# Kernel optimization log

Measured on AMD Instinct MI355X. Metric: run time of the kernel, lower is better.

Reference implementation:

```python
import jax, jax.numpy as jnp
import numpy as np

EPS = 1e-12  # F.normalize default eps
TOPK = 3

def _l2norm_c(x):
    # normalize over channel axis 1 of [b,c,h,w]
    n = jnp.sqrt(jnp.sum(x * x, axis=1, keepdims=True))
    return x / jnp.maximum(n, EPS)

def _topk_axis1(x, k):
    # torch.topk(x, k, dim=-3) on [b, N, h, w] -> values [b, k, h, w]
    t = jnp.moveaxis(x, 1, -1)            # [b,h,w,N]
    vals, _ = jax.lax.top_k(t, k)         # [b,h,w,k]
    return jnp.moveaxis(vals, -1, 1)      # [b,k,h,w]

def setup_inputs() -> dict:
    key = jax.random.key(0)
    k1, k2 = jax.random.split(key)
    b, c, h, w = 4, 256, 64, 64
    xp = jax.random.normal(k1, (b, c, h, w), dtype=jnp.float32)
    xq = jax.random.normal(k2, (b, c, h, w), dtype=jnp.float32)
    alpha = jnp.float32(10.0)  # learned scalar parameter
    return {"xp": xp, "xq": xq, "alpha": alpha}

def reference(xp, xq, alpha):
    b, c, h1, w1 = xp.shape
    _, _, h2, w2 = xq.shape
    xpn = _l2norm_c(xp)
    xqn = _l2norm_c(xq)
    # [b, h1*w1, c] @ [b, c, h2*w2] -> [b, N1, N2]
    p = jnp.transpose(xpn, (0, 2, 3, 1)).reshape(b, h1 * w1, c)
    q = xqn.reshape(b, c, h2 * w2)
    x_aff = jnp.matmul(p, q)
    s = x_aff * alpha
    x_c = jax.nn.softmax(s, axis=-1) * jax.nn.softmax(s, axis=-2)
    # row-major reshape matches torch .view semantics
    xc_o_q = x_c.reshape(b, h1 * w1, h2, w2)
    valq = _topk_axis1(xc_o_q, TOPK)
    xc_o_p = jnp.moveaxis(xc_o_q, 1, -1).reshape(b, h2 * w2, h1, w1)
    valp = _topk_axis1(xc_o_p, TOPK)
    return (valp, valq, xc_o_p, xc_o_q)
```

## Files before the change

kernel.cpp:

```cpp
#include <hip/hip_runtime.h>
#include <cstdint>
#include <cstddef>

#define B_ 4
#define C_ 256
#define N_ 4096
#define BN_TOT (B_ * N_)

typedef _Float16 f16x8 __attribute__((ext_vector_type(8)));
typedef _Float16 f16x4 __attribute__((ext_vector_type(4)));
typedef float f32x4 __attribute__((ext_vector_type(4)));

__global__ __launch_bounds__(256) void norms_kernel(const float* __restrict__ xp,
                                                    const float* __restrict__ xq,
                                                    float* __restrict__ invp,
                                                    float* __restrict__ invq) {
  int idx = blockIdx.x * 256 + threadIdx.x;
  int tensor = idx >> 14;
  int rem = idx & 16383;
  const float* p = (tensor ? xq : xp) + (size_t)(rem >> 12) * C_ * N_ + (rem & 4095);
  float ss = 0.f;
#pragma unroll 16
  for (int ch = 0; ch < C_; ++ch) {
    float v = p[(size_t)ch * N_];
    ss = fmaf(v, v, ss);
  }
  float inv = 1.0f / fmaxf(sqrtf(ss), 1e-12f);
  (tensor ? invq : invp)[rem] = inv;
}

__global__ __launch_bounds__(256) void convert_kernel(const float* __restrict__ xp,
                                                      const float* __restrict__ xq,
                                                      const float* __restrict__ invp,
                                                      const float* __restrict__ invq,
                                                      _Float16* __restrict__ ph,
                                                      _Float16* __restrict__ pl,
                                                      _Float16* __restrict__ qh,
                                                      _Float16* __restrict__ ql) {
  __shared__ _Float16 ht[64][72];
  __shared__ _Float16 lt[64][72];
  const int tensor = blockIdx.z & 1;
  const int b = blockIdx.z >> 1;
  const int i0 = blockIdx.x * 64;
  const int c0 = blockIdx.y * 64;
  const int tid = threadIdx.x;
  const int si = tid & 15;
  const int sc = tid >> 4;
  const float* x = (tensor ? xq : xp) + (size_t)b * C_ * N_;
  const float* inv = (tensor ? invq : invp) + b * N_;
  _Float16* oh = (tensor ? qh : ph) + (size_t)b * N_ * C_;
  _Float16* ol = (tensor ? ql : pl) + (size_t)b * N_ * C_;

  float4 iv = *(const float4*)&inv[i0 + si * 4];

  _Float16 hv[4][4], lv[4][4];
#pragma unroll
  for (int rr = 0; rr < 4; ++rr) {
    float4 v = *(const float4*)&x[(size_t)(c0 + sc * 4 + rr) * N_ + i0 + si * 4];
    float f0 = v.x * iv.x, f1 = v.y * iv.y, f2 = v.z * iv.z, f3 = v.w * iv.w;
    _Float16 h0 = (_Float16)f0, h1 = (_Float16)f1, h2 = (_Float16)f2, h3 = (_Float16)f3;
    hv[rr][0] = h0; lv[rr][0] = (_Float16)((f0 - (float)h0) * 1024.f);
    hv[rr][1] = h1; lv[rr][1] = (_Float16)((f1 - (float)h1) * 1024.f);
    hv[rr][2] = h2; lv[rr][2] = (_Float16)((f2 - (float)h2) * 1024.f);
    hv[rr][3] = h3; lv[rr][3] = (_Float16)((f3 - (float)h3) * 1024.f);
  }
#pragma unroll
  for (int u = 0; u < 4; ++u) {
    f16x4 th = {hv[0][u], hv[1][u], hv[2][u], hv[3][u]};
    f16x4 tl = {lv[0][u], lv[1][u], lv[2][u], lv[3][u]};
    *(f16x4*)&ht[si * 4 + u][sc * 4] = th;
    *(f16x4*)&lt[si * 4 + u][sc * 4] = tl;
  }
  __syncthreads();
  const int ir = tid >> 2;
  const int ch = tid & 3;
  f16x8 h0 = *(const f16x8*)&ht[ir][ch * 16];
  f16x8 h1 = *(const f16x8*)&ht[ir][ch * 16 + 8];
  f16x8 l0 = *(const f16x8*)&lt[ir][ch * 16];
  f16x8 l1 = *(const f16x8*)&lt[ir][ch * 16 + 8];
  _Float16* po = oh + (size_t)(i0 + ir) * C_ + c0 + ch * 16;
  *(f16x8*)po = h0;
  *(f16x8*)(po + 8) = h1;
  _Float16* po2 = ol + (size_t)(i0 + ir) * C_ + c0 + ch * 16;
  *(f16x8*)po2 = l0;
  *(f16x8*)(po2 + 8) = l1;
}

__global__ __launch_bounds__(256, 2) void gemm_mfma_kernel(
    const _Float16* __restrict__ ph, const _Float16* __restrict__ pl,
    const _Float16* __restrict__ qh, const _Float16* __restrict__ ql,
    const float* __restrict__ alpha_p,
    float* __restrict__ e_out,
    float* __restrict__ rowsum, float* __restrict__ colsum) {
  __shared__ _Float16 Ah[128][40];
  __shared__ _Float16 Al[128][40];
  __shared__ _Float16 Bh[128][40];
  __shared__ _Float16 Bl[128][40];
  __shared__ float redr[2][128];
  __shared__ float redc[2][128];

  const int b = blockIdx.z;
  const int i0 = blockIdx.y * 128;
  const int j0 = blockIdx.x * 128;
  const int tid = threadIdx.x;
  const int lane = tid & 63;
  const int wave = tid >> 6;
  const int wr = wave >> 1;
  const int wc = wave & 1;

  const size_t tb = (size_t)b * N_ * C_;
  const _Float16* pAh = ph + tb + (size_t)(i0 + (tid >> 1)) * C_ + (tid & 1) * 16;
  const _Float16* pAl = pl + tb + (size_t)(i0 + (tid >> 1)) * C_ + (tid & 1) * 16;
  const _Float16* pBh = qh + tb + (size_t)(j0 + (tid >> 1)) * C_ + (tid & 1) * 16;
  const _Float16* pBl = ql + tb + (size_t)(j0 + (tid >> 1)) * C_ + (tid & 1) * 16;

  _Float16* wAh = &Ah[tid >> 1][(tid & 1) * 16];
  _Float16* wAl = &Al[tid >> 1][(tid & 1) * 16];
  _Float16* wBh = &Bh[tid >> 1][(tid & 1) * 16];
  _Float16* wBl = &Bl[tid >> 1][(tid & 1) * 16];

  f32x4 acc_hh[4][4], acc_m[4][4];
#pragma unroll
  for (int m = 0; m < 4; ++m)
#pragma unroll
    for (int n = 0; n < 4; ++n) {
      acc_hh[m][n] = (f32x4){0.f, 0.f, 0.f, 0.f};
      acc_m[m][n] = (f32x4){0.f, 0.f, 0.f, 0.f};
    }

  const int frow = lane & 15;
  const int fk = (lane >> 4) * 8;

  for (int k0 = 0; k0 < C_; k0 += 32) {
    f16x8 ra0 = *(const f16x8*)(pAh + k0);
    f16x8 ra1 = *(const f16x8*)(pAh + k0 + 8);
    f16x8 rb0 = *(const f16x8*)(pAl + k0);
    f16x8 rb1 = *(const f16x8*)(pAl + k0 + 8);
    f16x8 rc0 = *(const f16x8*)(pBh + k0);
    f16x8 rc1 = *(const f16x8*)(pBh + k0 + 8);
    f16x8 rd0 = *(const f16x8*)(pBl + k0);
    f16x8 rd1 = *(const f16x8*)(pBl + k0 + 8);
    __syncthreads();
    *(f16x8*)wAh = ra0; *(f16x8*)(wAh + 8) = ra1;
    *(f16x8*)wAl = rb0; *(f16x8*)(wAl + 8) = rb1;
    *(f16x8*)wBh = rc0; *(f16x8*)(wBh + 8) = rc1;
    *(f16x8*)wBl = rd0; *(f16x8*)(wBl + 8) = rd1;
    __syncthreads();

    f16x8 fah[4], fal[4], fbh[4], fbl[4];
#pragma unroll
    for (int m = 0; m < 4; ++m) {
      fah[m] = *(const f16x8*)&Ah[wr * 64 + m * 16 + frow][fk];
      fal[m] = *(const f16x8*)&Al[wr * 64 + m * 16 + frow][fk];
    }
#pragma unroll
    for (int n = 0; n < 4; ++n) {
      fbh[n] = *(const f16x8*)&Bh[wc * 64 + n * 16 + frow][fk];
      fbl[n] = *(const f16x8*)&Bl[wc * 64 + n * 16 + frow][fk];
    }
#pragma unroll
    for (int m = 0; m < 4; ++m)
#pragma unroll
      for (int n = 0; n < 4; ++n) {
        acc_hh[m][n] = __builtin_amdgcn_mfma_f32_16x16x32_f16(fah[m], fbh[n], acc_hh[m][n], 0, 0, 0);
        acc_m[m][n]  = __builtin_amdgcn_mfma_f32_16x16x32_f16(fah[m], fbl[n], acc_m[m][n], 0, 0, 0);
        acc_m[m][n]  = __builtin_amdgcn_mfma_f32_16x16x32_f16(fal[m], fbh[n], acc_m[m][n], 0, 0, 0);
      }
  }

  const float al = alpha_p[0];
  float rowp[4][4];
  float colp[4];
#pragma unroll
  for (int m = 0; m < 4; ++m)
#pragma unroll
    for (int r = 0; r < 4; ++r) rowp[m][r] = 0.f;
#pragma unroll
  for (int n = 0; n < 4; ++n) colp[n] = 0.f;

  const int rbase = i0 + wr * 64;
  const int cbase = j0 + wc * 64;
  const int rlane = (lane >> 4) * 4;
  const int clane = lane & 15;

#pragma unroll
  for (int m = 0; m < 4; ++m)
#pragma unroll
    for (int n = 0; n < 4; ++n) {
      f32x4 dh = acc_hh[m][n];
      f32x4 dm = acc_m[m][n];
#pragma unroll
      for (int reg = 0; reg < 4; ++reg) {
        float dot = dh[reg] + dm[reg] * (1.f / 1024.f);
        float e = __expf(al * dot);
        int row = rbase + m * 16 + rlane + reg;
        int col = cbase + n * 16 + clane;
        e_out[(size_t)(b * N_ + row) * N_ + col] = e;
        rowp[m][reg] += e;
        colp[n] += e;
      }
    }

#pragma unroll
  for (int m = 0; m < 4; ++m)
#pragma unroll
    for (int reg = 0; reg < 4; ++reg) {
      float r = rowp[m][reg];
      r += __shfl_xor(r, 1);
      r += __shfl_xor(r, 2);
      r += __shfl_xor(r, 4);
      r += __shfl_xor(r, 8);
      if (clane == 0) redr[wc][wr * 64 + m * 16 + rlane + reg] = r;
    }
#pragma unroll
  for (int n = 0; n < 4; ++n) {
    float c = colp[n];
    c += __shfl_xor(c, 16);
    c += __shfl_xor(c, 32);
    if (lane < 16) redc[wr][wc * 64 + n * 16 + clane] = c;
  }
  __syncthreads();
  if (tid < 128) {
    atomicAdd(&rowsum[b * N_ + i0 + tid], redr[0][tid] + redr[1][tid]);
    atomicAdd(&colsum[b * N_ + j0 + tid], redc[0][tid] + redc[1][tid]);
  }
}

__global__ __launch_bounds__(256) void recip_kernel(float* __restrict__ v) {
  int idx = blockIdx.x * 256 + threadIdx.x;
  v[idx] = 1.0f / v[idx];
}

__device__ __forceinline__ void top3_insert(float& a0, float& a1, float& a2, float x) {
  float m0 = fmaxf(a0, x);
  float c0 = fminf(a0, x);
  float m1 = fmaxf(a1, c0);
  float c1 = fminf(a1, c0);
  float m2 = fmaxf(a2, c1);
  a0 = m0; a1 = m1; a2 = m2;
}

__global__ __launch_bounds__(256) void finalize_kernel(float* __restrict__ eq,
                                                       float* __restrict__ outp,
                                                       const float* __restrict__ invr,
                                                       const float* __restrict__ invc,
                                                       float* __restrict__ rowpart,
                                                       float* __restrict__ colpart) {
  __shared__ float t[64][65];
  __shared__ float cpart[4][64][3];

  const int b = blockIdx.z;
  const int i0 = blockIdx.y * 64;
  const int j0 = blockIdx.x * 64;
  const int tid = threadIdx.x;
  const int tr = tid >> 4;
  const int tc = (tid & 15) << 2;
  const int wave = tid >> 6;
  const int lane = tid & 63;

  float ic0 = invc[b * N_ + j0 + tc + 0];
  float ic1 = invc[b * N_ + j0 + tc + 1];
  float ic2 = invc[b * N_ + j0 + tc + 2];
  float ic3 = invc[b * N_ + j0 + tc + 3];

  float c0a[4], c1a[4], c2a[4];
#pragma unroll
  for (int c = 0; c < 4; ++c) { c0a[c] = -1e30f; c1a[c] = -1e30f; c2a[c] = -1e30f; }

  const size_t basq = (size_t)(b * N_ + i0) * N_ + j0;
#pragma unroll
  for (int rg = 0; rg < 4; ++rg) {
    const int li = rg * 16 + tr;
    const float ir = invr[b * N_ + i0 + li];
    float4 e4 = *(const float4*)(eq + basq + (size_t)li * N_ + tc);
    float4 v;
    v.x = e4.x * e4.x * ir * ic0;
    v.y = e4.y * e4.y * ir * ic1;
    v.z = e4.z * e4.z * ir * ic2;
    v.w = e4.w * e4.w * ir * ic3;
    *(float4*)(eq + basq + (size_t)li * N_ + tc) = v;
    t[tc + 0][li] = v.x;
    t[tc + 1][li] = v.y;
    t[tc + 2][li] = v.z;
    t[tc + 3][li] = v.w;

    float r0 = -1e30f, r1 = -1e30f, r2 = -1e30f;
    top3_insert(r0, r1, r2, v.x);
    top3_insert(r0, r1, r2, v.y);
    top3_insert(r0, r1, r2, v.z);
    top3_insert(r0, r1, r2, v.w);
#pragma unroll
    for (int mask = 1; mask <= 8; mask <<= 1) {
      float b0 = __shfl_xor(r0, mask);
      float b1 = __shfl_xor(r1, mask);
      float b2 = __shfl_xor(r2, mask);
      top3_insert(r0, r1, r2, b0);
      top3_insert(r0, r1, r2, b1);
      top3_insert(r0, r1, r2, b2);
    }
    if ((tid & 15) == 0) {
      const size_t rb = ((size_t)(b * 64 + (j0 >> 6)) * 3) * N_ + i0 + li;
      rowpart[rb] = r0;
      rowpart[rb + N_] = r1;
      rowpart[rb + 2 * (size_t)N_] = r2;
    }

    top3_insert(c0a[0], c1a[0], c2a[0], v.x);
    top3_insert(c0a[1], c1a[1], c2a[1], v.y);
    top3_insert(c0a[2], c1a[2], c2a[2], v.z);
    top3_insert(c0a[3], c1a[3], c2a[3], v.w);
  }

#pragma unroll
  for (int mask = 16; mask <= 32; mask <<= 1) {
#pragma unroll
    for (int c = 0; c < 4; ++c) {
      float b0 = __shfl_xor(c0a[c], mask);
      float b1 = __shfl_xor(c1a[c], mask);
      float b2 = __shfl_xor(c2a[c], mask);
      top3_insert(c0a[c], c1a[c], c2a[c], b0);
      top3_insert(c0a[c], c1a[c], c2a[c], b1);
      top3_insert(c0a[c], c1a[c], c2a[c], b2);
    }
  }
  if (lane < 16) {
#pragma unroll
    for (int c = 0; c < 4; ++c) {
      cpart[wave][tc + c][0] = c0a[c];
      cpart[wave][tc + c][1] = c1a[c];
      cpart[wave][tc + c][2] = c2a[c];
    }
  }

  __syncthreads();

  const size_t basp = (size_t)(b * N_ + j0) * N_ + i0;
#pragma unroll
  for (int cg = 0; cg < 4; ++cg) {
    const int lj = cg * 16 + tr;
    float4 v;
    v.x = t[lj][tc + 0];
    v.y = t[lj][tc + 1];
    v.z = t[lj][tc + 2];
    v.w = t[lj][tc + 3];
    *(float4*)(outp + basp + (size_t)lj * N_ + tc) = v;
  }

  if (tid < 64) {
    float a0 = -1e30f, a1 = -1e30f, a2 = -1e30f;
#pragma unroll
    for (int w = 0; w < 4; ++w) {
      top3_insert(a0, a1, a2, cpart[w][tid][0]);
      top3_insert(a0, a1, a2, cpart[w][tid][1]);
      top3_insert(a0, a1, a2, cpart[w][tid][2]);
    }
    const size_t cb = ((size_t)(b * 64 + (i0 >> 6)) * 3) * N_ + j0 + tid;
    colpart[cb] = a0;
    colpart[cb + N_] = a1;
    colpart[cb + 2 * (size_t)N_] = a2;
  }
}

__global__ __launch_bounds__(256) void top3_merge_kernel(const float* __restrict__ rowpart,
                                                         const float* __restrict__ colpart,
                                                         float* __restrict__ valp,
                                                         float* __restrict__ valq) {
  const int gid = blockIdx.x * 256 + threadIdx.x;
  const int which = gid >> 14;
  const int rem = gid & 16383;
  const int b = rem >> 12;
  const int r = rem & 4095;
  const float* part = (which ? colpart : rowpart) + (size_t)(b * 64) * 3 * N_ + r;

  float a0 = -1e30f, a1 = -1e30f, a2 = -1e30f;
#pragma unroll 4
  for (int t = 0; t < 192; ++t) {
    top3_insert(a0, a1, a2, part[0]);
    part += N_;
  }
  float* out = which ? valq : valp;
  out[(b * 3 + 0) * N_ + r] = a0;
  out[(b * 3 + 1) * N_ + r] = a1;
  out[(b * 3 + 2) * N_ + r] = a2;
}

extern "C" void kernel_launch(void* const* d_in, const int* in_sizes, int n_in,
                              void* d_out, int out_size, void* d_ws, size_t ws_size,
                              hipStream_t stream) {
  const float* xp = (const float*)d_in[0];
  const float* xq = (const float*)d_in[1];
  const float* alpha = (const float*)d_in[2];

  float* o = (float*)d_out;
  float* valp = o;
  float* valq = o + 49152;
  float* xcp = o + 98304;
  float* xcq = o + 98304 + 67108864;

  float* wsf = (float*)d_ws;
  float* invp = wsf;
  float* invq = wsf + 16384;
  float* rowsum = wsf + 32768;
  float* colsum = wsf + 49152;
  char* dyn = (char*)(wsf + 65536);
  _Float16* ph = (_Float16*)dyn;
  _Float16* pl = ph + (size_t)B_ * N_ * C_;
  _Float16* qh = pl + (size_t)B_ * N_ * C_;
  _Float16* ql = qh + (size_t)B_ * N_ * C_;
  float* rowpart = (float*)dyn;
  float* colpart = rowpart + 3145728;

  hipMemsetAsync(rowsum, 0, (size_t)2 * BN_TOT * sizeof(float), stream);

  norms_kernel<<<2 * BN_TOT / 256, 256, 0, stream>>>(xp, xq, invp, invq);

  convert_kernel<<<dim3(N_ / 64, C_ / 64, 2 * B_), 256, 0, stream>>>(
      xp, xq, invp, invq, ph, pl, qh, ql);

  gemm_mfma_kernel<<<dim3(N_ / 128, N_ / 128, B_), 256, 0, stream>>>(
      ph, pl, qh, ql, alpha, xcq, rowsum, colsum);

  recip_kernel<<<2 * BN_TOT / 256, 256, 0, stream>>>(rowsum);

  finalize_kernel<<<dim3(N_ / 64, N_ / 64, B_), 256, 0, stream>>>(
      xcq, xcp, rowsum, colsum, rowpart, colpart);

  top3_merge_kernel<<<2 * BN_TOT / 256, 256, 0, stream>>>(rowpart, colpart, valp, valq);
}
```

Before: 836.5 us.

## Fuse norms into convert, double-buffer GEMM LDS, remap blocks, nontemporal stores

```diff
diff --git a/kernel.cpp b/kernel.cpp
--- a/kernel.cpp
+++ b/kernel.cpp
@@ -11,97 +11,114 @@
 typedef _Float16 f16x4 __attribute__((ext_vector_type(4)));
 typedef float f32x4 __attribute__((ext_vector_type(4)));
 
-__global__ __launch_bounds__(256) void norms_kernel(const float* __restrict__ xp,
-                                                    const float* __restrict__ xq,
-                                                    float* __restrict__ invp,
-                                                    float* __restrict__ invq) {
-  int idx = blockIdx.x * 256 + threadIdx.x;
-  int tensor = idx >> 14;
-  int rem = idx & 16383;
-  const float* p = (tensor ? xq : xp) + (size_t)(rem >> 12) * C_ * N_ + (rem & 4095);
-  float ss = 0.f;
-#pragma unroll 16
-  for (int ch = 0; ch < C_; ++ch) {
-    float v = p[(size_t)ch * N_];
-    ss = fmaf(v, v, ss);
-  }
-  float inv = 1.0f / fmaxf(sqrtf(ss), 1e-12f);
-  (tensor ? invq : invp)[rem] = inv;
-}
-
 __global__ __launch_bounds__(256) void convert_kernel(const float* __restrict__ xp,
                                                       const float* __restrict__ xq,
-                                                      const float* __restrict__ invp,
-                                                      const float* __restrict__ invq,
                                                       _Float16* __restrict__ ph,
                                                       _Float16* __restrict__ pl,
                                                       _Float16* __restrict__ qh,
                                                       _Float16* __restrict__ ql) {
   __shared__ _Float16 ht[64][72];
   __shared__ _Float16 lt[64][72];
+  __shared__ float red[16][64];
+  __shared__ float invs[64];
   const int tensor = blockIdx.z & 1;
   const int b = blockIdx.z >> 1;
   const int i0 = blockIdx.x * 64;
-  const int c0 = blockIdx.y * 64;
   const int tid = threadIdx.x;
   const int si = tid & 15;
   const int sc = tid >> 4;
   const float* x = (tensor ? xq : xp) + (size_t)b * C_ * N_;
-  const float* inv = (tensor ? invq : invp) + b * N_;
   _Float16* oh = (tensor ? qh : ph) + (size_t)b * N_ * C_;
   _Float16* ol = (tensor ? ql : pl) + (size_t)b * N_ * C_;
 
-  float4 iv = *(const float4*)&inv[i0 + si * 4];
-
-  _Float16 hv[4][4], lv[4][4];
-#pragma unroll
-  for (int rr = 0; rr < 4; ++rr) {
-    float4 v = *(const float4*)&x[(size_t)(c0 + sc * 4 + rr) * N_ + i0 + si * 4];
-    float f0 = v.x * iv.x, f1 = v.y * iv.y, f2 = v.z * iv.z, f3 = v.w * iv.w;
-    _Float16 h0 = (_Float16)f0, h1 = (_Float16)f1, h2 = (_Float16)f2, h3 = (_Float16)f3;
-    hv[rr][0] = h0; lv[rr][0] = (_Float16)((f0 - (float)h0) * 1024.f);
-    hv[rr][1] = h1; lv[rr][1] = (_Float16)((f1 - (float)h1) * 1024.f);
-    hv[rr][2] = h2; lv[rr][2] = (_Float16)((f2 - (float)h2) * 1024.f);
-    hv[rr][3] = h3; lv[rr][3] = (_Float16)((f3 - (float)h3) * 1024.f);
-  }
-#pragma unroll
-  for (int u = 0; u < 4; ++u) {
-    f16x4 th = {hv[0][u], hv[1][u], hv[2][u], hv[3][u]};
-    f16x4 tl = {lv[0][u], lv[1][u], lv[2][u], lv[3][u]};
-    *(f16x4*)&ht[si * 4 + u][sc * 4] = th;
-    *(f16x4*)&lt[si * 4 + u][sc * 4] = tl;
-  }
+  float4 data[4][4];
+  float ss0 = 0.f, ss1 = 0.f, ss2 = 0.f, ss3 = 0.f;
+#pragma unroll
+  for (int cb = 0; cb < 4; ++cb)
+#pragma unroll
+    for (int rr = 0; rr < 4; ++rr) {
+      float4 v = *(const float4*)&x[(size_t)(cb * 64 + sc * 4 + rr) * N_ + i0 + si * 4];
+      data[cb][rr] = v;
+      ss0 = fmaf(v.x, v.x, ss0);
+      ss1 = fmaf(v.y, v.y, ss1);
+      ss2 = fmaf(v.z, v.z, ss2);
+      ss3 = fmaf(v.w, v.w, ss3);
+    }
+  red[sc][si * 4 + 0] = ss0;
+  red[sc][si * 4 + 1] = ss1;
+  red[sc][si * 4 + 2] = ss2;
+  red[sc][si * 4 + 3] = ss3;
   __syncthreads();
-  const int ir = tid >> 2;
-  const int ch = tid & 3;
-  f16x8 h0 = *(const f16x8*)&ht[ir][ch * 16];
-  f16x8 h1 = *(const f16x8*)&ht[ir][ch * 16 + 8];
-  f16x8 l0 = *(const f16x8*)&lt[ir][ch * 16];
-  f16x8 l1 = *(const f16x8*)&lt[ir][ch * 16 + 8];
-  _Float16* po = oh + (size_t)(i0 + ir) * C_ + c0 + ch * 16;
-  *(f16x8*)po = h0;
-  *(f16x8*)(po + 8) = h1;
-  _Float16* po2 = ol + (size_t)(i0 + ir) * C_ + c0 + ch * 16;
-  *(f16x8*)po2 = l0;
-  *(f16x8*)(po2 + 8) = l1;
-}
-
+  if (tid < 64) {
+    float s = 0.f;
+#pragma unroll
+    for (int w = 0; w < 16; ++w) s += red[w][tid];
+    invs[tid] = 1.0f / fmaxf(sqrtf(s), 1e-12f);
+  }
+  __syncthreads();
+  const float iv0 = invs[si * 4 + 0];
+  const float iv1 = invs[si * 4 + 1];
+  const float iv2 = invs[si * 4 + 2];
+  const float iv3 = invs[si * 4 + 3];
+
+#pragma unroll
+  for (int cb = 0; cb < 4; ++cb) {
+    _Float16 hv[4][4], lv[4][4];
+#pragma unroll
+    for (int rr = 0; rr < 4; ++rr) {
+      float4 v = data[cb][rr];
+      float f0 = v.x * iv0, f1 = v.y * iv1, f2 = v.z * iv2, f3 = v.w * iv3;
+      _Float16 h0 = (_Float16)f0, h1 = (_Float16)f1, h2 = (_Float16)f2, h3 = (_Float16)f3;
+      hv[rr][0] = h0; lv[rr][0] = (_Float16)((f0 - (float)h0) * 1024.f);
+      hv[rr][1] = h1; lv[rr][1] = (_Float16)((f1 - (float)h1) * 1024.f);
+      hv[rr][2] = h2; lv[rr][2] = (_Float16)((f2 - (float)h2) * 1024.f);
+      hv[rr][3] = h3; lv[rr][3] = (_Float16)((f3 - (float)h3) * 1024.f);
+    }
+#pragma unroll
+    for (int u = 0; u < 4; ++u) {
+      f16x4 th = {hv[0][u], hv[1][u], hv[2][u], hv[3][u]};
+      f16x4 tl = {lv[0][u], lv[1][u], lv[2][u], lv[3][u]};
+      *(f16x4*)&ht[si * 4 + u][sc * 4] = th;
+      *(f16x4*)&lt[si * 4 + u][sc * 4] = tl;
+    }
+    __syncthreads();
+    const int ir = tid >> 2;
+    const int ch = tid & 3;
+    f16x8 h0 = *(const f16x8*)&ht[ir][ch * 16];
+    f16x8 h1 = *(const f16x8*)&ht[ir][ch * 16 + 8];
+    f16x8 l0 = *(const f16x8*)&lt[ir][ch * 16];
+    f16x8 l1 = *(const f16x8*)&lt[ir][ch * 16 + 8];
+    _Float16* po = oh + (size_t)(i0 + ir) * C_ + cb * 64 + ch * 16;
+    *(f16x8*)po = h0;
+    *(f16x8*)(po + 8) = h1;
+    _Float16* po2 = ol + (size_t)(i0 + ir) * C_ + cb * 64 + ch * 16;
+    *(f16x8*)po2 = l0;
+    *(f16x8*)(po2 + 8) = l1;
+    __syncthreads();
+  }
+}
+
+#define PADK 36
 __global__ __launch_bounds__(256, 2) void gemm_mfma_kernel(
     const _Float16* __restrict__ ph, const _Float16* __restrict__ pl,
     const _Float16* __restrict__ qh, const _Float16* __restrict__ ql,
     const float* __restrict__ alpha_p,
     float* __restrict__ e_out,
     float* __restrict__ rowsum, float* __restrict__ colsum) {
-  __shared__ _Float16 Ah[128][40];
-  __shared__ _Float16 Al[128][40];
-  __shared__ _Float16 Bh[128][40];
-  __shared__ _Float16 Bl[128][40];
+  __shared__ _Float16 Ah[2][128][PADK];
+  __shared__ _Float16 Al[2][128][PADK];
+  __shared__ _Float16 Bh[2][128][PADK];
+  __shared__ _Float16 Bl[2][128][PADK];
   __shared__ float redr[2][128];
   __shared__ float redc[2][128];
 
-  const int b = blockIdx.z;
-  const int i0 = blockIdx.y * 128;
-  const int j0 = blockIdx.x * 128;
+  const int lin = blockIdx.x + 32 * blockIdx.y + 1024 * blockIdx.z;
+  const int nid = (lin & 7) * 512 + (lin >> 3);
+  const int b = nid >> 10;
+  const int rest = nid & 1023;
+  const int j0 = (rest & 31) * 128;
+  const int i0 = ((rest >> 5) & 31) * 128;
+
   const int tid = threadIdx.x;
   const int lane = tid & 63;
   const int wave = tid >> 6;
@@ -109,15 +126,12 @@
   const int wc = wave & 1;
 
   const size_t tb = (size_t)b * N_ * C_;
-  const _Float16* pAh = ph + tb + (size_t)(i0 + (tid >> 1)) * C_ + (tid & 1) * 16;
-  const _Float16* pAl = pl + tb + (size_t)(i0 + (tid >> 1)) * C_ + (tid & 1) * 16;
-  const _Float16* pBh = qh + tb + (size_t)(j0 + (tid >> 1)) * C_ + (tid & 1) * 16;
-  const _Float16* pBl = ql + tb + (size_t)(j0 + (tid >> 1)) * C_ + (tid & 1) * 16;
-
-  _Float16* wAh = &Ah[tid >> 1][(tid & 1) * 16];
-  _Float16* wAl = &Al[tid >> 1][(tid & 1) * 16];
-  _Float16* wBh = &Bh[tid >> 1][(tid & 1) * 16];
-  _Float16* wBl = &Bl[tid >> 1][(tid & 1) * 16];
+  const int srow = tid >> 1;
+  const int scol = (tid & 1) * 16;
+  const _Float16* gAh = ph + tb + (size_t)(i0 + srow) * C_ + scol;
+  const _Float16* gAl = pl + tb + (size_t)(i0 + srow) * C_ + scol;
+  const _Float16* gBh = qh + tb + (size_t)(j0 + srow) * C_ + scol;
+  const _Float16* gBl = ql + tb + (size_t)(j0 + srow) * C_ + scol;
 
   f32x4 acc_hh[4][4], acc_m[4][4];
 #pragma unroll
@@ -129,43 +143,67 @@
     }
 
   const int frow = lane & 15;
-  const int fk = (lane >> 4) * 8;
-
-  for (int k0 = 0; k0 < C_; k0 += 32) {
-    f16x8 ra0 = *(const f16x8*)(pAh + k0);
-    f16x8 ra1 = *(const f16x8*)(pAh + k0 + 8);
-    f16x8 rb0 = *(const f16x8*)(pAl + k0);
-    f16x8 rb1 = *(const f16x8*)(pAl + k0 + 8);
-    f16x8 rc0 = *(const f16x8*)(pBh + k0);
-    f16x8 rc1 = *(const f16x8*)(pBh + k0 + 8);
-    f16x8 rd0 = *(const f16x8*)(pBl + k0);
-    f16x8 rd1 = *(const f16x8*)(pBl + k0 + 8);
+  const int fko = (lane >> 4) * 8;
+
+  {
+    f16x8 ra0 = *(const f16x8*)(gAh);
+    f16x8 ra1 = *(const f16x8*)(gAh + 8);
+    f16x8 rb0 = *(const f16x8*)(gAl);
+    f16x8 rb1 = *(const f16x8*)(gAl + 8);
+    f16x8 rc0 = *(const f16x8*)(gBh);
+    f16x8 rc1 = *(const f16x8*)(gBh + 8);
+    f16x8 rd0 = *(const f16x8*)(gBl);
+    f16x8 rd1 = *(const f16x8*)(gBl + 8);
+    *(f16x8*)&Ah[0][srow][scol] = ra0; *(f16x8*)&Ah[0][srow][scol + 8] = ra1;
+    *(f16x8*)&Al[0][srow][scol] = rb0; *(f16x8*)&Al[0][srow][scol + 8] = rb1;
+    *(f16x8*)&Bh[0][srow][scol] = rc0; *(f16x8*)&Bh[0][srow][scol + 8] = rc1;
+    *(f16x8*)&Bl[0][srow][scol] = rd0; *(f16x8*)&Bl[0][srow][scol + 8] = rd1;
+  }
+
+  int buf = 0;
+  for (int t = 0; t < 8; ++t) {
+    f16x8 ra0, ra1, rb0, rb1, rc0, rc1, rd0, rd1;
+    if (t < 7) {
+      const int ko = (t + 1) * 32;
+      ra0 = *(const f16x8*)(gAh + ko);
+      ra1 = *(const f16x8*)(gAh + ko + 8);
+      rb0 = *(const f16x8*)(gAl + ko);
+      rb1 = *(const f16x8*)(gAl + ko + 8);
+      rc0 = *(const f16x8*)(gBh + ko);
+      rc1 = *(const f16x8*)(gBh + ko + 8);
+      rd0 = *(const f16x8*)(gBl + ko);
+      rd1 = *(const f16x8*)(gBl + ko + 8);
+    }
     __syncthreads();
-    *(f16x8*)wAh = ra0; *(f16x8*)(wAh + 8) = ra1;
-    *(f16x8*)wAl = rb0; *(f16x8*)(wAl + 8) = rb1;
-    *(f16x8*)wBh = rc0; *(f16x8*)(wBh + 8) = rc1;
-    *(f16x8*)wBl = rd0; *(f16x8*)(wBl + 8) = rd1;
-    __syncthreads();
-
-    f16x8 fah[4], fal[4], fbh[4], fbl[4];
+
+    f16x8 fah[4], fal[4];
 #pragma unroll
     for (int m = 0; m < 4; ++m) {
-      fah[m] = *(const f16x8*)&Ah[wr * 64 + m * 16 + frow][fk];
-      fal[m] = *(const f16x8*)&Al[wr * 64 + m * 16 + frow][fk];
-    }
+      fah[m] = *(const f16x8*)&Ah[buf][wr * 64 + m * 16 + frow][fko];
+      fal[m] = *(const f16x8*)&Al[buf][wr * 64 + m * 16 + frow][fko];
+    }
+    __builtin_amdgcn_s_setprio(1);
 #pragma unroll
     for (int n = 0; n < 4; ++n) {
-      fbh[n] = *(const f16x8*)&Bh[wc * 64 + n * 16 + frow][fk];
-      fbl[n] = *(const f16x8*)&Bl[wc * 64 + n * 16 + frow][fk];
-    }
-#pragma unroll
-    for (int m = 0; m < 4; ++m)
-#pragma unroll
-      for (int n = 0; n < 4; ++n) {
-        acc_hh[m][n] = __builtin_amdgcn_mfma_f32_16x16x32_f16(fah[m], fbh[n], acc_hh[m][n], 0, 0, 0);
-        acc_m[m][n]  = __builtin_amdgcn_mfma_f32_16x16x32_f16(fah[m], fbl[n], acc_m[m][n], 0, 0, 0);
-        acc_m[m][n]  = __builtin_amdgcn_mfma_f32_16x16x32_f16(fal[m], fbh[n], acc_m[m][n], 0, 0, 0);
+      f16x8 fbh = *(const f16x8*)&Bh[buf][wc * 64 + n * 16 + frow][fko];
+      f16x8 fbl = *(const f16x8*)&Bl[buf][wc * 64 + n * 16 + frow][fko];
+#pragma unroll
+      for (int m = 0; m < 4; ++m) {
+        acc_hh[m][n] = __builtin_amdgcn_mfma_f32_16x16x32_f16(fah[m], fbh, acc_hh[m][n], 0, 0, 0);
+        acc_m[m][n]  = __builtin_amdgcn_mfma_f32_16x16x32_f16(fah[m], fbl, acc_m[m][n], 0, 0, 0);
+        acc_m[m][n]  = __builtin_amdgcn_mfma_f32_16x16x32_f16(fal[m], fbh, acc_m[m][n], 0, 0, 0);
       }
+    }
+    __builtin_amdgcn_s_setprio(0);
+
+    if (t < 7) {
+      const int nb = buf ^ 1;
+      *(f16x8*)&Ah[nb][srow][scol] = ra0; *(f16x8*)&Ah[nb][srow][scol + 8] = ra1;
+      *(f16x8*)&Al[nb][srow][scol] = rb0; *(f16x8*)&Al[nb][srow][scol + 8] = rb1;
+      *(f16x8*)&Bh[nb][srow][scol] = rc0; *(f16x8*)&Bh[nb][srow][scol + 8] = rc1;
+      *(f16x8*)&Bl[nb][srow][scol] = rd0; *(f16x8*)&Bl[nb][srow][scol + 8] = rd1;
+    }
+    buf ^= 1;
   }
 
   const float al = alpha_p[0];
@@ -273,12 +311,12 @@
     const int li = rg * 16 + tr;
     const float ir = invr[b * N_ + i0 + li];
     float4 e4 = *(const float4*)(eq + basq + (size_t)li * N_ + tc);
-    float4 v;
+    f32x4 v;
     v.x = e4.x * e4.x * ir * ic0;
     v.y = e4.y * e4.y * ir * ic1;
     v.z = e4.z * e4.z * ir * ic2;
     v.w = e4.w * e4.w * ir * ic3;
-    *(float4*)(eq + basq + (size_t)li * N_ + tc) = v;
+    __builtin_nontemporal_store(v, (f32x4*)(eq + basq + (size_t)li * N_ + tc));
     t[tc + 0][li] = v.x;
     t[tc + 1][li] = v.y;
     t[tc + 2][li] = v.z;
@@ -338,12 +376,12 @@
 #pragma unroll
   for (int cg = 0; cg < 4; ++cg) {
     const int lj = cg * 16 + tr;
-    float4 v;
+    f32x4 v;
     v.x = t[lj][tc + 0];
     v.y = t[lj][tc + 1];
     v.z = t[lj][tc + 2];
     v.w = t[lj][tc + 3];
-    *(float4*)(outp + basp + (size_t)lj * N_ + tc) = v;
+    __builtin_nontemporal_store(v, (f32x4*)(outp + basp + (size_t)lj * N_ + tc));
   }
 
   if (tid < 64) {
@@ -398,8 +436,6 @@
   float* xcq = o + 98304 + 67108864;
 
   float* wsf = (float*)d_ws;
-  float* invp = wsf;
-  float* invq = wsf + 16384;
   float* rowsum = wsf + 32768;
   float* colsum = wsf + 49152;
   char* dyn = (char*)(wsf + 65536);
@@ -410,12 +446,10 @@
   float* rowpart = (float*)dyn;
   float* colpart = rowpart + 3145728;
 
-  hipMemsetAsync(rowsum, 0, (size_t)2 * BN_TOT * sizeof(float), stream);
-
-  norms_kernel<<<2 * BN_TOT / 256, 256, 0, stream>>>(xp, xq, invp, invq);
-
-  convert_kernel<<<dim3(N_ / 64, C_ / 64, 2 * B_), 256, 0, stream>>>(
-      xp, xq, invp, invq, ph, pl, qh, ql);
+  (void)hipMemsetAsync(rowsum, 0, (size_t)2 * BN_TOT * sizeof(float), stream);
+
+  convert_kernel<<<dim3(N_ / 64, 1, 2 * B_), 256, 0, stream>>>(
+      xp, xq, ph, pl, qh, ql);
 
   gemm_mfma_kernel<<<dim3(N_ / 128, N_ / 128, B_), 256, 0, stream>>>(
       ph, pl, qh, ql, alpha, xcq, rowsum, colsum);
```

After: 785.7 us. 6.1% less time.
